# Kernel optimization log

Hardware: AMD Instinct MI355X
Metric: run time of the kernel (lower is better)

## Reference

```python
import jax, jax.numpy as jnp
import numpy as np

N = 100000
E = 1600000
D_IN = 128
HID = 128
OUT = 64


def _sage_conv(x, edge_index, W_l, W_r, b, num_nodes):
    # PyG SAGEConv (aggr='mean'): out = lin_l(mean_{j in N(i)} x_j) + lin_r(x_i)
    src, dst = edge_index[0], edge_index[1]
    msgs = x[src]  # [E, d] gather from source nodes
    summed = jax.ops.segment_sum(msgs, dst, num_segments=num_nodes)  # [N, d]
    cnt = jax.ops.segment_sum(jnp.ones((msgs.shape[0],), x.dtype), dst, num_segments=num_nodes)
    agg = summed / jnp.maximum(cnt, 1.0)[:, None]  # mean; isolated nodes -> 0
    return agg @ W_l + b + x @ W_r


def setup_inputs() -> dict:
    key = jax.random.key(0)
    ks = jax.random.split(key, 8)
    x = jax.random.normal(ks[0], (N, D_IN), dtype=jnp.float32)
    edge_index = jax.random.randint(ks[1], (2, E), 0, N, dtype=jnp.int64)
    s1 = 1.0 / np.sqrt(D_IN)
    s2 = 1.0 / np.sqrt(HID)
    W_l1 = jax.random.uniform(ks[2], (D_IN, HID), jnp.float32, -s1, s1)
    W_r1 = jax.random.uniform(ks[3], (D_IN, HID), jnp.float32, -s1, s1)
    b1 = jnp.zeros((HID,), jnp.float32)
    W_l2 = jax.random.uniform(ks[4], (HID, OUT), jnp.float32, -s2, s2)
    W_r2 = jax.random.uniform(ks[5], (HID, OUT), jnp.float32, -s2, s2)
    b2 = jnp.zeros((OUT,), jnp.float32)
    return {"x": x, "edge_index": edge_index, "W_l1": W_l1, "W_r1": W_r1,
            "b1": b1, "W_l2": W_l2, "W_r2": W_r2, "b2": b2}


def reference(x, edge_index, W_l1, W_r1, b1, W_l2, W_r2, b2):
    h = _sage_conv(x, edge_index, W_l1, W_r1, b1, N)
    h = jax.nn.relu(h)
    out = _sage_conv(h, edge_index, W_l2, W_r2, b2, N)
    return out
```

## Files before the change

kernel.cpp:

```cpp
#include <hip/hip_runtime.h>
#include <hip/hip_fp16.h>

typedef __attribute__((ext_vector_type(8))) short bf16x8;
typedef __attribute__((ext_vector_type(4))) float f32x4;

__device__ __forceinline__ f32x4 mfma16(bf16x8 a, bf16x8 b, f32x4 c) {
    return __builtin_amdgcn_mfma_f32_16x16x32_bf16(a, b, c, 0, 0, 0);
}

__device__ __forceinline__ unsigned short bf16_rte(float f) {
    unsigned int u = __float_as_uint(f);
    unsigned int r = (u + 0x7FFFu + ((u >> 16) & 1u)) >> 16;
    return (unsigned short)r;
}
__device__ __forceinline__ float bf16_f(unsigned short h) {
    return __uint_as_float(((unsigned int)h) << 16);
}

__device__ __forceinline__ void split8h(bf16x8 raw, bf16x8& hi, bf16x8& lo) {
#pragma unroll
    for (int j = 0; j < 8; ++j) {
        float f = __half2float(__ushort_as_half((unsigned short)raw[j]));
        unsigned short h = bf16_rte(f);
        hi[j] = (short)h;
        lo[j] = (short)bf16_rte(f - bf16_f(h));
    }
}

__global__ __launch_bounds__(256) void k_wconv_all(
    const float* __restrict__ Wl1, const float* __restrict__ Wr1,
    const float* __restrict__ Wl2, const float* __restrict__ Wr2,
    unsigned short* __restrict__ w1ah, unsigned short* __restrict__ w1al,
    unsigned short* __restrict__ w1bh, unsigned short* __restrict__ w1bl,
    unsigned short* __restrict__ w2ah, unsigned short* __restrict__ w2al,
    unsigned short* __restrict__ w2bh, unsigned short* __restrict__ w2bl) {
    int b = blockIdx.x;
    const float* W;
    unsigned short *hi, *lo;
    int F, e;
    if (b < 64)       { W = Wl1; hi = w1ah; lo = w1al; F = 128; e = b * 256 + threadIdx.x; }
    else if (b < 128) { W = Wr1; hi = w1bh; lo = w1bl; F = 128; e = (b - 64) * 256 + threadIdx.x; }
    else if (b < 160) { W = Wl2; hi = w2ah; lo = w2al; F = 64;  e = (b - 128) * 256 + threadIdx.x; }
    else              { W = Wr2; hi = w2bh; lo = w2bl; F = 64;  e = (b - 160) * 256 + threadIdx.x; }
    if (e >= 128 * F) return;
    int col = e >> 7, k = e & 127;
    float v = W[(size_t)k * F + col];
    unsigned short h = bf16_rte(v);
    hi[e] = h;
    lo[e] = bf16_rte(v - bf16_f(h));
}

__global__ __launch_bounds__(256) void k_xconv(const float* __restrict__ x,
                                               unsigned short* __restrict__ x16,
                                               int total8) {
    int i = blockIdx.x * 256 + threadIdx.x;
    if (i >= total8) return;
    const float4* xp = (const float4*)x + (size_t)i * 2;
    float4 a = xp[0], b = xp[1];
    bf16x8 o;
    o[0] = (short)__half_as_ushort(__float2half_rn(a.x));
    o[1] = (short)__half_as_ushort(__float2half_rn(a.y));
    o[2] = (short)__half_as_ushort(__float2half_rn(a.z));
    o[3] = (short)__half_as_ushort(__float2half_rn(a.w));
    o[4] = (short)__half_as_ushort(__float2half_rn(b.x));
    o[5] = (short)__half_as_ushort(__float2half_rn(b.y));
    o[6] = (short)__half_as_ushort(__float2half_rn(b.z));
    o[7] = (short)__half_as_ushort(__float2half_rn(b.w));
    *(bf16x8*)&x16[(size_t)i * 8] = o;
}


#define MAXNB 1024

__global__ __launch_bounds__(256) void k_bcount(
    const int* __restrict__ dst, int* __restrict__ bcnt, int E, int chunk, int nb) {
    __shared__ int h[MAXNB];
    int t = threadIdx.x;
    for (int i = t; i < nb; i += 256) h[i] = 0;
    __syncthreads();
    int base = blockIdx.x * chunk;
    int end = min(base + chunk, E);
    for (int i = base + t; i < end; i += 256) atomicAdd(&h[dst[i] >> 7], 1);
    __syncthreads();
    for (int i = t; i < nb; i += 256)
        if (h[i]) atomicAdd(&bcnt[i], h[i]);
}

__global__ void k_bscan(const int* __restrict__ bcnt, int* __restrict__ boff,
                        int* __restrict__ bcur, int nb) {
    __shared__ int sh[1024];
    int t = threadIdx.x;
    int v = (t < nb) ? bcnt[t] : 0;
    sh[t] = v;
    __syncthreads();
    for (int off = 1; off < 1024; off <<= 1) {
        int u = (t >= off) ? sh[t - off] : 0;
        __syncthreads();
        sh[t] += u;
        __syncthreads();
    }
    if (t < nb) {
        int ex = sh[t] - v;
        boff[t] = ex;
        bcur[t] = ex;
    }
}

__global__ __launch_bounds__(256) void k_bscatter(
    const int* __restrict__ src, const int* __restrict__ dst,
    int* __restrict__ bcur, int2* __restrict__ pairs, int E, int chunk, int nb) {
    __shared__ int h[MAXNB];
    __shared__ int curs[MAXNB];
    int t = threadIdx.x;
    for (int i = t; i < nb; i += 256) h[i] = 0;
    __syncthreads();
    int base = blockIdx.x * chunk;
    int end = min(base + chunk, E);
    for (int i = base + t; i < end; i += 256) atomicAdd(&h[dst[i] >> 7], 1);
    __syncthreads();
    for (int i = t; i < nb; i += 256)
        curs[i] = h[i] ? atomicAdd(&bcur[i], h[i]) : 0;
    __syncthreads();
    for (int i = base + t; i < end; i += 256) {
        int d = dst[i];
        int p = atomicAdd(&curs[d >> 7], 1);
        pairs[p] = make_int2(d, src[i]);
    }
}

__global__ __launch_bounds__(256) void k_build(
    const int2* __restrict__ pairs, const int* __restrict__ boff,
    int* __restrict__ csr, int* __restrict__ start, int* __restrict__ deg,
    int n, int nb, int E) {
    __shared__ int scnt[128];
    __shared__ int soff[128];
    __shared__ int cur[128];
    int b = blockIdx.x;
    int t = threadIdx.x;
    int base = boff[b];
    int end = (b + 1 < nb) ? boff[b + 1] : E;
    if (t < 128) scnt[t] = 0;
    __syncthreads();
    for (int i = base + t; i < end; i += 256) {
        int2 e = pairs[i];
        atomicAdd(&scnt[e.x & 127], 1);
    }
    __syncthreads();
    if (t < 128) soff[t] = scnt[t];
    __syncthreads();
    for (int off = 1; off < 128; off <<= 1) {
        int val = 0;
        if (t < 128 && t >= off) val = soff[t - off];
        __syncthreads();
        if (t < 128) soff[t] += val;
        __syncthreads();
    }
    if (t < 128) {
        int c = scnt[t];
        int ex = soff[t] - c;
        int node = b * 128 + t;
        if (node < n) {
            start[node] = base + ex;
            deg[node] = c;
        }
        cur[t] = base + ex;
    }
    __syncthreads();
    for (int i = base + t; i < end; i += 256) {
        int2 e = pairs[i];
        int p = atomicAdd(&cur[e.x & 127], 1);
        csr[p] = e.y;
    }
}


#define SR 40

template <int FOUT, bool OUT_H16>
__device__ __forceinline__ void gemm_dual_body(
    const unsigned short* __restrict__ X0h, const unsigned short* __restrict__ X1h,
    const unsigned short* __restrict__ W0H, const unsigned short* __restrict__ W0L,
    const unsigned short* __restrict__ W1H, const unsigned short* __restrict__ W1L,
    const float* __restrict__ bias, unsigned short* __restrict__ dstH,
    float* __restrict__ dstF, int n) {
    constexpr int CT = FOUT / 64;
    __shared__ unsigned short aHi[4][64 * SR], aLo[4][64 * SR];

    int t = threadIdx.x;
    int wv = t >> 6, l = t & 63, q = l >> 4, nl = l & 15;
    int wc = wv * (FOUT / 4);
    int node0 = blockIdx.x * 64;
    int sn = t >> 2, q4 = t & 3;
    int gn = min(node0 + sn, n - 1);

    bf16x8 s1r[4];
    {
        const unsigned short* p = X1h + (size_t)gn * 128 + q4 * 8;
#pragma unroll
        for (int c = 0; c < 4; ++c) s1r[c] = *(const bf16x8*)(p + c * 32);
    }
    bf16x8 w1h0[CT], w1l0[CT];
#pragma unroll
    for (int uu = 0; uu < CT; ++uu) {
        int base = (wc + uu * 16 + nl) * 128 + q * 8;
        w1h0[uu] = *(const bf16x8*)&W1H[base];
        w1l0[uu] = *(const bf16x8*)&W1L[base];
    }

    {
        const unsigned short* p = X0h + (size_t)gn * 128 + q4 * 8;
        bf16x8 r[4];
#pragma unroll
        for (int c = 0; c < 4; ++c) r[c] = *(const bf16x8*)(p + c * 32);
        int base = sn * SR + q4 * 8;
#pragma unroll
        for (int c = 0; c < 4; ++c) {
            bf16x8 hi, lo;
            split8h(r[c], hi, lo);
            *(bf16x8*)&aHi[c][base] = hi;
            *(bf16x8*)&aLo[c][base] = lo;
        }
    }

    f32x4 acc[4][CT];
#pragma unroll
    for (int a = 0; a < 4; ++a)
#pragma unroll
        for (int b = 0; b < CT; ++b) acc[a][b] = (f32x4){0.f, 0.f, 0.f, 0.f};

    bf16x8 wh[2][CT], wl[2][CT];
#pragma unroll
    for (int uu = 0; uu < CT; ++uu) {
        int base = (wc + uu * 16 + nl) * 128 + q * 8;
        wh[0][uu] = *(const bf16x8*)&W0H[base];
        wl[0][uu] = *(const bf16x8*)&W0L[base];
    }
    __syncthreads();

#pragma unroll
    for (int c = 0; c < 4; ++c) {
        if (c < 3) {
#pragma unroll
            for (int uu = 0; uu < CT; ++uu) {
                int base = (wc + uu * 16 + nl) * 128 + (c + 1) * 32 + q * 8;
                wh[(c + 1) & 1][uu] = *(const bf16x8*)&W0H[base];
                wl[(c + 1) & 1][uu] = *(const bf16x8*)&W0L[base];
            }
        }
        bf16x8 ah[4], al[4];
#pragma unroll
        for (int tt = 0; tt < 4; ++tt) {
            int off = (tt * 16 + nl) * SR + q * 8;
            ah[tt] = *(const bf16x8*)&aHi[c][off];
            al[tt] = *(const bf16x8*)&aLo[c][off];
        }
        int cb = c & 1;
#pragma unroll
        for (int tt = 0; tt < 4; ++tt)
#pragma unroll
            for (int uu = 0; uu < CT; ++uu) {
                f32x4 a = acc[tt][uu];
                a = mfma16(al[tt], wh[cb][uu], a);
                a = mfma16(ah[tt], wl[cb][uu], a);
                a = mfma16(ah[tt], wh[cb][uu], a);
                acc[tt][uu] = a;
            }
    }
    __syncthreads();

    {
        int base = sn * SR + q4 * 8;
#pragma unroll
        for (int c = 0; c < 4; ++c) {
            bf16x8 hi, lo;
            split8h(s1r[c], hi, lo);
            *(bf16x8*)&aHi[c][base] = hi;
            *(bf16x8*)&aLo[c][base] = lo;
        }
    }
#pragma unroll
    for (int uu = 0; uu < CT; ++uu) { wh[0][uu] = w1h0[uu]; wl[0][uu] = w1l0[uu]; }
    __syncthreads();

#pragma unroll
    for (int c = 0; c < 4; ++c) {
        if (c < 3) {
#pragma unroll
            for (int uu = 0; uu < CT; ++uu) {
                int base = (wc + uu * 16 + nl) * 128 + (c + 1) * 32 + q * 8;
                wh[(c + 1) & 1][uu] = *(const bf16x8*)&W1H[base];
                wl[(c + 1) & 1][uu] = *(const bf16x8*)&W1L[base];
            }
        }
        bf16x8 ah[4], al[4];
#pragma unroll
        for (int tt = 0; tt < 4; ++tt) {
            int off = (tt * 16 + nl) * SR + q * 8;
            ah[tt] = *(const bf16x8*)&aHi[c][off];
            al[tt] = *(const bf16x8*)&aLo[c][off];
        }
        int cb = c & 1;
#pragma unroll
        for (int tt = 0; tt < 4; ++tt)
#pragma unroll
            for (int uu = 0; uu < CT; ++uu) {
                f32x4 a = acc[tt][uu];
                a = mfma16(al[tt], wh[cb][uu], a);
                a = mfma16(ah[tt], wl[cb][uu], a);
                a = mfma16(ah[tt], wh[cb][uu], a);
                acc[tt][uu] = a;
            }
    }
    __syncthreads();

    if (OUT_H16) {
        unsigned short* tb = &aHi[0][0];
#pragma unroll
        for (int uu = 0; uu < CT; ++uu) {
            int col = wc + uu * 16 + nl;
            float bv = bias[col];
#pragma unroll
            for (int tt = 0; tt < 4; ++tt)
#pragma unroll
                for (int r = 0; r < 4; ++r) {
                    float vv = fmaxf(acc[tt][uu][r] + bv, 0.f);
                    tb[(tt * 16 + q * 4 + r) * 136 + col] =
                        __half_as_ushort(__float2half_rn(vv));
                }
        }
        __syncthreads();
        int node = node0 + sn;
        if (node < n) {
            const unsigned short* sp = tb + sn * 136 + q4 * 32;
            unsigned short* dp = dstH + (size_t)node * 128 + q4 * 32;
#pragma unroll
            for (int i = 0; i < 4; ++i) *(bf16x8*)(dp + i * 8) = *(const bf16x8*)(sp + i * 8);
        }
    } else {
        float* tb = (float*)&aHi[0][0];
#pragma unroll
        for (int uu = 0; uu < CT; ++uu) {
            int col = wc + uu * 16 + nl;
            float bv = bias[col];
#pragma unroll
            for (int tt = 0; tt < 4; ++tt)
#pragma unroll
                for (int r = 0; r < 4; ++r)
                    tb[(tt * 16 + q * 4 + r) * 68 + col] = acc[tt][uu][r] + bv;
        }
        __syncthreads();
        int node = node0 + sn;
        if (node < n) {
            const float* sp = tb + sn * 68 + q4 * 16;
            float* dp = dstF + (size_t)node * 64 + q4 * 16;
#pragma unroll
            for (int i = 0; i < 4; ++i) *(float4*)(dp + i * 4) = *(const float4*)(sp + i * 4);
        }
    }
}

__global__ __launch_bounds__(256, 4) void gemm1f(
    const unsigned short* __restrict__ X, const unsigned short* __restrict__ XM,
    const unsigned short* WrH, const unsigned short* WrL,
    const unsigned short* WlH, const unsigned short* WlL,
    const float* __restrict__ bias, unsigned short* __restrict__ h16, int n) {
    gemm_dual_body<128, true>(X, XM, WrH, WrL, WlH, WlL, bias, h16, nullptr, n);
}

__global__ __launch_bounds__(256, 4) void gemm2f(
    const unsigned short* __restrict__ H, const unsigned short* __restrict__ HM,
    const unsigned short* WrH, const unsigned short* WrL,
    const unsigned short* WlH, const unsigned short* WlL,
    const float* __restrict__ bias, float* __restrict__ out, int n) {
    gemm_dual_body<64, false>(H, HM, WrH, WrL, WlH, WlL, bias, nullptr, out, n);
}

__global__ __launch_bounds__(256) void aggF(
    const unsigned short* __restrict__ tab, const int* __restrict__ csr,
    const int* __restrict__ start, const int* __restrict__ deg,
    unsigned short* __restrict__ outm, int n) {
    int gid = blockIdx.x * blockDim.x + threadIdx.x;
    int wave = gid >> 6, lane = gid & 63;
    int sub = lane >> 4, fl = lane & 15;
    int node = wave * 4 + sub;
    if (node >= n) return;
    int s = start[node], d = deg[node];
    float4 A0 = {0.f, 0.f, 0.f, 0.f}, A1 = {0.f, 0.f, 0.f, 0.f};
    int j = 0;
    if (d >= 4) {
        int i0 = csr[s], i1 = csr[s + 1], i2 = csr[s + 2], i3 = csr[s + 3];
        for (; j + 8 <= d; j += 4) {
            int n0 = csr[s + j + 4], n1 = csr[s + j + 5];
            int n2 = csr[s + j + 6], n3 = csr[s + j + 7];
            uint4 r0 = ((const uint4*)(tab + (size_t)i0 * 128))[fl];
            uint4 r1 = ((const uint4*)(tab + (size_t)i1 * 128))[fl];
            uint4 r2 = ((const uint4*)(tab + (size_t)i2 * 128))[fl];
            uint4 r3 = ((const uint4*)(tab + (size_t)i3 * 128))[fl];
#pragma unroll
            for (int e = 0; e < 4; ++e) {
                uint4 r = e == 0 ? r0 : (e == 1 ? r1 : (e == 2 ? r2 : r3));
                float2 v0 = __half22float2(*(const __half2*)&r.x);
                float2 v1 = __half22float2(*(const __half2*)&r.y);
                float2 v2 = __half22float2(*(const __half2*)&r.z);
                float2 v3 = __half22float2(*(const __half2*)&r.w);
                A0.x += v0.x; A0.y += v0.y; A0.z += v1.x; A0.w += v1.y;
                A1.x += v2.x; A1.y += v2.y; A1.z += v3.x; A1.w += v3.y;
            }
            i0 = n0; i1 = n1; i2 = n2; i3 = n3;
        }
        {
            uint4 r0 = ((const uint4*)(tab + (size_t)i0 * 128))[fl];
            uint4 r1 = ((const uint4*)(tab + (size_t)i1 * 128))[fl];
            uint4 r2 = ((const uint4*)(tab + (size_t)i2 * 128))[fl];
            uint4 r3 = ((const uint4*)(tab + (size_t)i3 * 128))[fl];
#pragma unroll
            for (int e = 0; e < 4; ++e) {
                uint4 r = e == 0 ? r0 : (e == 1 ? r1 : (e == 2 ? r2 : r3));
                float2 v0 = __half22float2(*(const __half2*)&r.x);
                float2 v1 = __half22float2(*(const __half2*)&r.y);
                float2 v2 = __half22float2(*(const __half2*)&r.z);
                float2 v3 = __half22float2(*(const __half2*)&r.w);
                A0.x += v0.x; A0.y += v0.y; A0.z += v1.x; A0.w += v1.y;
                A1.x += v2.x; A1.y += v2.y; A1.z += v3.x; A1.w += v3.y;
            }
            j += 4;
        }
    }
    for (; j < d; ++j) {
        uint4 r = ((const uint4*)(tab + (size_t)csr[s + j] * 128))[fl];
        float2 v0 = __half22float2(*(const __half2*)&r.x);
        float2 v1 = __half22float2(*(const __half2*)&r.y);
        float2 v2 = __half22float2(*(const __half2*)&r.z);
        float2 v3 = __half22float2(*(const __half2*)&r.w);
        A0.x += v0.x; A0.y += v0.y; A0.z += v1.x; A0.w += v1.y;
        A1.x += v2.x; A1.y += v2.y; A1.z += v3.x; A1.w += v3.y;
    }
    float inv = 1.0f / (float)max(d, 1);
    __half2 h0 = __floats2half2_rn(A0.x * inv, A0.y * inv);
    __half2 h1 = __floats2half2_rn(A0.z * inv, A0.w * inv);
    __half2 h2 = __floats2half2_rn(A1.x * inv, A1.y * inv);
    __half2 h3 = __floats2half2_rn(A1.z * inv, A1.w * inv);
    uint4 w;
    w.x = *(unsigned int*)&h0;
    w.y = *(unsigned int*)&h1;
    w.z = *(unsigned int*)&h2;
    w.w = *(unsigned int*)&h3;
    *(uint4*)&outm[(size_t)node * 128 + fl * 8] = w;
}


extern "C" void kernel_launch(void* const* d_in, const int* in_sizes, int n_in,
                              void* d_out, int out_size, void* d_ws, size_t ws_size,
                              hipStream_t stream) {
    const float* x   = (const float*)d_in[0];
    const int*   ei  = (const int*)d_in[1];
    const float* Wl1 = (const float*)d_in[2];
    const float* Wr1 = (const float*)d_in[3];
    const float* b1  = (const float*)d_in[4];
    const float* Wl2 = (const float*)d_in[5];
    const float* Wr2 = (const float*)d_in[6];
    const float* b2  = (const float*)d_in[7];
    float* out = (float*)d_out;

    int Nn = in_sizes[0] / 128;
    int E  = in_sizes[1] / 2;
    const int* src = ei;
    const int* dst = ei + E;
    int nb = (Nn + 127) / 128;

    char* ws = (char*)d_ws;
    auto alloc = [&](size_t bytes) -> char* {
        char* pp = ws;
        ws += (bytes + 255) / 256 * 256;
        return pp;
    };
    int* bcnt   = (int*)alloc((size_t)nb * 4);
    int* boff   = (int*)alloc((size_t)nb * 4);
    int* bcur   = (int*)alloc((size_t)nb * 4);
    int* start  = (int*)alloc((size_t)Nn * 4);
    int* deg    = (int*)alloc((size_t)Nn * 4);
    int* csr    = (int*)alloc((size_t)E * 4);
    unsigned short* x16  = (unsigned short*)alloc((size_t)Nn * 128 * 2);
    unsigned short* xm16 = (unsigned short*)alloc((size_t)Nn * 128 * 2);
    unsigned short* h16  = (unsigned short*)alloc((size_t)Nn * 128 * 2);
    unsigned short* hm16 = (unsigned short*)alloc((size_t)Nn * 128 * 2);
    unsigned short* w1ah = (unsigned short*)alloc(128 * 128 * 2);
    unsigned short* w1al = (unsigned short*)alloc(128 * 128 * 2);
    unsigned short* w1bh = (unsigned short*)alloc(128 * 128 * 2);
    unsigned short* w1bl = (unsigned short*)alloc(128 * 128 * 2);
    unsigned short* w2ah = (unsigned short*)alloc(64 * 128 * 2);
    unsigned short* w2al = (unsigned short*)alloc(64 * 128 * 2);
    unsigned short* w2bh = (unsigned short*)alloc(64 * 128 * 2);
    unsigned short* w2bl = (unsigned short*)alloc(64 * 128 * 2);
    int2* pairs = (int2*)hm16;

    hipMemsetAsync(bcnt, 0, (size_t)nb * 4, stream);

    k_wconv_all<<<192, 256, 0, stream>>>(Wl1, Wr1, Wl2, Wr2,
                                         w1ah, w1al, w1bh, w1bl,
                                         w2ah, w2al, w2bh, w2bl);
    k_xconv<<<(Nn * 16 + 255) / 256, 256, 0, stream>>>(x, x16, Nn * 16);

    int chunk = (E + 255) / 256;
    k_bcount<<<256, 256, 0, stream>>>(dst, bcnt, E, chunk, nb);
    k_bscan<<<1, 1024, 0, stream>>>(bcnt, boff, bcur, nb);
    k_bscatter<<<256, 256, 0, stream>>>(src, dst, bcur, pairs, E, chunk, nb);
    k_build<<<nb, 256, 0, stream>>>(pairs, boff, csr, start, deg, Nn, nb, E);

    int gb = (Nn + 63) / 64;
    int ga = (Nn + 15) / 16;
    aggF<<<ga, 256, 0, stream>>>(x16, csr, start, deg, xm16, Nn);
    gemm1f<<<gb, 256, 0, stream>>>(x16, xm16, w1bh, w1bl, w1ah, w1al, b1, h16, Nn);
    aggF<<<ga, 256, 0, stream>>>(h16, csr, start, deg, hm16, Nn);
    gemm2f<<<gb, 256, 0, stream>>>(h16, hm16, w2bh, w2bl, w2ah, w2al, b2, out, Nn);
}
```

Measured before the change: 366.8 us.

## Project layer-2 features before aggregation and fuse prep kernels

Layer 2 now multiplies h by W_l2 first (a 64-wide fp16 table) and by W_r2 plus the bias, then averages the projected 64-wide rows over neighbours and adds them to the output. This uses the linearity of the mean so the second gather reads 64 fp16 features per edge instead of 128. The weight conversion, x conversion and bcnt zeroing are merged into one launch, and the GEMM launch bounds drop from 4 to 2 blocks per unit. In exchange the projected values are rounded to fp16 before averaging, and the output gets a read-modify-write pass.

```diff
diff --git a/kernel.cpp b/kernel.cpp
--- a/kernel.cpp
+++ b/kernel.cpp
@@ -27,46 +27,49 @@
     }
 }
 
-__global__ __launch_bounds__(256) void k_wconv_all(
+__global__ __launch_bounds__(256) void k_prep(
     const float* __restrict__ Wl1, const float* __restrict__ Wr1,
     const float* __restrict__ Wl2, const float* __restrict__ Wr2,
     unsigned short* __restrict__ w1ah, unsigned short* __restrict__ w1al,
     unsigned short* __restrict__ w1bh, unsigned short* __restrict__ w1bl,
     unsigned short* __restrict__ w2ah, unsigned short* __restrict__ w2al,
-    unsigned short* __restrict__ w2bh, unsigned short* __restrict__ w2bl) {
+    unsigned short* __restrict__ w2bh, unsigned short* __restrict__ w2bl,
+    const float* __restrict__ x, unsigned short* __restrict__ x16,
+    int* __restrict__ bcnt, int nb, int total8) {
     int b = blockIdx.x;
-    const float* W;
-    unsigned short *hi, *lo;
-    int F, e;
-    if (b < 64)       { W = Wl1; hi = w1ah; lo = w1al; F = 128; e = b * 256 + threadIdx.x; }
-    else if (b < 128) { W = Wr1; hi = w1bh; lo = w1bl; F = 128; e = (b - 64) * 256 + threadIdx.x; }
-    else if (b < 160) { W = Wl2; hi = w2ah; lo = w2al; F = 64;  e = (b - 128) * 256 + threadIdx.x; }
-    else              { W = Wr2; hi = w2bh; lo = w2bl; F = 64;  e = (b - 160) * 256 + threadIdx.x; }
-    if (e >= 128 * F) return;
-    int col = e >> 7, k = e & 127;
-    float v = W[(size_t)k * F + col];
-    unsigned short h = bf16_rte(v);
-    hi[e] = h;
-    lo[e] = bf16_rte(v - bf16_f(h));
-}
-
-__global__ __launch_bounds__(256) void k_xconv(const float* __restrict__ x,
-                                               unsigned short* __restrict__ x16,
-                                               int total8) {
-    int i = blockIdx.x * 256 + threadIdx.x;
-    if (i >= total8) return;
-    const float4* xp = (const float4*)x + (size_t)i * 2;
-    float4 a = xp[0], b = xp[1];
-    bf16x8 o;
-    o[0] = (short)__half_as_ushort(__float2half_rn(a.x));
-    o[1] = (short)__half_as_ushort(__float2half_rn(a.y));
-    o[2] = (short)__half_as_ushort(__float2half_rn(a.z));
-    o[3] = (short)__half_as_ushort(__float2half_rn(a.w));
-    o[4] = (short)__half_as_ushort(__float2half_rn(b.x));
-    o[5] = (short)__half_as_ushort(__float2half_rn(b.y));
-    o[6] = (short)__half_as_ushort(__float2half_rn(b.z));
-    o[7] = (short)__half_as_ushort(__float2half_rn(b.w));
-    *(bf16x8*)&x16[(size_t)i * 8] = o;
+    int t = threadIdx.x;
+    if (b < 192) {
+        const float* W;
+        unsigned short *hi, *lo;
+        int F, e;
+        if (b < 64)       { W = Wl1; hi = w1ah; lo = w1al; F = 128; e = b * 256 + t; }
+        else if (b < 128) { W = Wr1; hi = w1bh; lo = w1bl; F = 128; e = (b - 64) * 256 + t; }
+        else if (b < 160) { W = Wl2; hi = w2ah; lo = w2al; F = 64;  e = (b - 128) * 256 + t; }
+        else              { W = Wr2; hi = w2bh; lo = w2bl; F = 64;  e = (b - 160) * 256 + t; }
+        if (e >= 128 * F) return;
+        int col = e >> 7, k = e & 127;
+        float v = W[(size_t)k * F + col];
+        unsigned short h = bf16_rte(v);
+        hi[e] = h;
+        lo[e] = bf16_rte(v - bf16_f(h));
+    } else if (b == 192) {
+        for (int i = t; i < nb; i += 256) bcnt[i] = 0;
+    } else {
+        int i = (b - 193) * 256 + t;
+        if (i >= total8) return;
+        const float4* xp = (const float4*)x + (size_t)i * 2;
+        float4 a = xp[0], bb = xp[1];
+        bf16x8 o;
+        o[0] = (short)__half_as_ushort(__float2half_rn(a.x));
+        o[1] = (short)__half_as_ushort(__float2half_rn(a.y));
+        o[2] = (short)__half_as_ushort(__float2half_rn(a.z));
+        o[3] = (short)__half_as_ushort(__float2half_rn(a.w));
+        o[4] = (short)__half_as_ushort(__float2half_rn(bb.x));
+        o[5] = (short)__half_as_ushort(__float2half_rn(bb.y));
+        o[6] = (short)__half_as_ushort(__float2half_rn(bb.z));
+        o[7] = (short)__half_as_ushort(__float2half_rn(bb.w));
+        *(bf16x8*)&x16[(size_t)i * 8] = o;
+    }
 }
 
 
@@ -176,14 +179,13 @@
 
 #define SR 40
 
-template <int FOUT, bool OUT_H16>
-__device__ __forceinline__ void gemm_dual_body(
+__global__ __launch_bounds__(256, 2) void gemm1f(
     const unsigned short* __restrict__ X0h, const unsigned short* __restrict__ X1h,
     const unsigned short* __restrict__ W0H, const unsigned short* __restrict__ W0L,
     const unsigned short* __restrict__ W1H, const unsigned short* __restrict__ W1L,
-    const float* __restrict__ bias, unsigned short* __restrict__ dstH,
-    float* __restrict__ dstF, int n) {
-    constexpr int CT = FOUT / 64;
+    const float* __restrict__ bias, unsigned short* __restrict__ dstH, int n) {
+    constexpr int FOUT = 128;
+    constexpr int CT = 2;
     __shared__ unsigned short aHi[4][64 * SR], aLo[4][64 * SR];
 
     int t = threadIdx.x;
@@ -313,66 +315,143 @@
     }
     __syncthreads();
 
-    if (OUT_H16) {
-        unsigned short* tb = &aHi[0][0];
-#pragma unroll
-        for (int uu = 0; uu < CT; ++uu) {
-            int col = wc + uu * 16 + nl;
+    unsigned short* tb = &aHi[0][0];
+#pragma unroll
+    for (int uu = 0; uu < CT; ++uu) {
+        int col = wc + uu * 16 + nl;
+        float bv = bias[col];
+#pragma unroll
+        for (int tt = 0; tt < 4; ++tt)
+#pragma unroll
+            for (int r = 0; r < 4; ++r) {
+                float vv = fmaxf(acc[tt][uu][r] + bv, 0.f);
+                tb[(tt * 16 + q * 4 + r) * 136 + col] =
+                    __half_as_ushort(__float2half_rn(vv));
+            }
+    }
+    __syncthreads();
+    int node = node0 + sn;
+    if (node < n) {
+        const unsigned short* sp = tb + sn * 136 + q4 * 32;
+        unsigned short* dp = dstH + (size_t)node * 128 + q4 * 32;
+#pragma unroll
+        for (int i = 0; i < 4; ++i) *(bf16x8*)(dp + i * 8) = *(const bf16x8*)(sp + i * 8);
+    }
+}
+
+__global__ __launch_bounds__(256, 2) void gemm2d(
+    const unsigned short* __restrict__ H,
+    const unsigned short* __restrict__ WaH, const unsigned short* __restrict__ WaL,
+    const unsigned short* __restrict__ WbH, const unsigned short* __restrict__ WbL,
+    const float* __restrict__ bias, unsigned short* __restrict__ p16,
+    float* __restrict__ outF, int n) {
+    constexpr int CT = 2;
+    __shared__ unsigned short aHi[4][64 * SR], aLo[4][64 * SR];
+
+    int t = threadIdx.x;
+    int wv = t >> 6, l = t & 63, q = l >> 4, nl = l & 15;
+    int ysel = wv >> 1;
+    int wc = (wv & 1) * 32;
+    int node0 = blockIdx.x * 64;
+    int sn = t >> 2, q4 = t & 3;
+    int gn = min(node0 + sn, n - 1);
+    const unsigned short* WH = ysel ? WbH : WaH;
+    const unsigned short* WL = ysel ? WbL : WaL;
+
+    {
+        const unsigned short* p = H + (size_t)gn * 128 + q4 * 8;
+        bf16x8 r[4];
+#pragma unroll
+        for (int c = 0; c < 4; ++c) r[c] = *(const bf16x8*)(p + c * 32);
+        int base = sn * SR + q4 * 8;
+#pragma unroll
+        for (int c = 0; c < 4; ++c) {
+            bf16x8 hi, lo;
+            split8h(r[c], hi, lo);
+            *(bf16x8*)&aHi[c][base] = hi;
+            *(bf16x8*)&aLo[c][base] = lo;
+        }
+    }
+
+    f32x4 acc[4][CT];
+#pragma unroll
+    for (int a = 0; a < 4; ++a)
+#pragma unroll
+        for (int b = 0; b < CT; ++b) acc[a][b] = (f32x4){0.f, 0.f, 0.f, 0.f};
+
+    bf16x8 wh[2][CT], wl[2][CT];
+#pragma unroll
+    for (int uu = 0; uu < CT; ++uu) {
+        int base = (wc + uu * 16 + nl) * 128 + q * 8;
+        wh[0][uu] = *(const bf16x8*)&WH[base];
+        wl[0][uu] = *(const bf16x8*)&WL[base];
+    }
+    __syncthreads();
+
+#pragma unroll
+    for (int c = 0; c < 4; ++c) {
+        if (c < 3) {
+#pragma unroll
+            for (int uu = 0; uu < CT; ++uu) {
+                int base = (wc + uu * 16 + nl) * 128 + (c + 1) * 32 + q * 8;
+                wh[(c + 1) & 1][uu] = *(const bf16x8*)&WH[base];
+                wl[(c + 1) & 1][uu] = *(const bf16x8*)&WL[base];
+            }
+        }
+        bf16x8 ah[4], al[4];
+#pragma unroll
+        for (int tt = 0; tt < 4; ++tt) {
+            int off = (tt * 16 + nl) * SR + q * 8;
+            ah[tt] = *(const bf16x8*)&aHi[c][off];
+            al[tt] = *(const bf16x8*)&aLo[c][off];
+        }
+        int cb = c & 1;
+#pragma unroll
+        for (int tt = 0; tt < 4; ++tt)
+#pragma unroll
+            for (int uu = 0; uu < CT; ++uu) {
+                f32x4 a = acc[tt][uu];
+                a = mfma16(al[tt], wh[cb][uu], a);
+                a = mfma16(ah[tt], wl[cb][uu], a);
+                a = mfma16(ah[tt], wh[cb][uu], a);
+                acc[tt][uu] = a;
+            }
+    }
+    __syncthreads();
+
+    unsigned short* tbu = &aHi[0][0];
+    float* tbf = (float*)&aLo[0][0];
+#pragma unroll
+    for (int uu = 0; uu < CT; ++uu) {
+        int col = wc + uu * 16 + nl;
+        if (ysel) {
             float bv = bias[col];
 #pragma unroll
             for (int tt = 0; tt < 4; ++tt)
 #pragma unroll
-                for (int r = 0; r < 4; ++r) {
-                    float vv = fmaxf(acc[tt][uu][r] + bv, 0.f);
-                    tb[(tt * 16 + q * 4 + r) * 136 + col] =
-                        __half_as_ushort(__float2half_rn(vv));
-                }
-        }
-        __syncthreads();
-        int node = node0 + sn;
-        if (node < n) {
-            const unsigned short* sp = tb + sn * 136 + q4 * 32;
-            unsigned short* dp = dstH + (size_t)node * 128 + q4 * 32;
-#pragma unroll
-            for (int i = 0; i < 4; ++i) *(bf16x8*)(dp + i * 8) = *(const bf16x8*)(sp + i * 8);
-        }
-    } else {
-        float* tb = (float*)&aHi[0][0];
-#pragma unroll
-        for (int uu = 0; uu < CT; ++uu) {
-            int col = wc + uu * 16 + nl;
-            float bv = bias[col];
+                for (int r = 0; r < 4; ++r)
+                    tbf[(tt * 16 + q * 4 + r) * 68 + col] = acc[tt][uu][r] + bv;
+        } else {
 #pragma unroll
             for (int tt = 0; tt < 4; ++tt)
 #pragma unroll
                 for (int r = 0; r < 4; ++r)
-                    tb[(tt * 16 + q * 4 + r) * 68 + col] = acc[tt][uu][r] + bv;
-        }
-        __syncthreads();
-        int node = node0 + sn;
-        if (node < n) {
-            const float* sp = tb + sn * 68 + q4 * 16;
-            float* dp = dstF + (size_t)node * 64 + q4 * 16;
-#pragma unroll
-            for (int i = 0; i < 4; ++i) *(float4*)(dp + i * 4) = *(const float4*)(sp + i * 4);
-        }
-    }
-}
-
-__global__ __launch_bounds__(256, 4) void gemm1f(
-    const unsigned short* __restrict__ X, const unsigned short* __restrict__ XM,
-    const unsigned short* WrH, const unsigned short* WrL,
-    const unsigned short* WlH, const unsigned short* WlL,
-    const float* __restrict__ bias, unsigned short* __restrict__ h16, int n) {
-    gemm_dual_body<128, true>(X, XM, WrH, WrL, WlH, WlL, bias, h16, nullptr, n);
-}
-
-__global__ __launch_bounds__(256, 4) void gemm2f(
-    const unsigned short* __restrict__ H, const unsigned short* __restrict__ HM,
-    const unsigned short* WrH, const unsigned short* WrL,
-    const unsigned short* WlH, const unsigned short* WlL,
-    const float* __restrict__ bias, float* __restrict__ out, int n) {
-    gemm_dual_body<64, false>(H, HM, WrH, WrL, WlH, WlL, bias, nullptr, out, n);
+                    tbu[(tt * 16 + q * 4 + r) * 72 + col] =
+                        __half_as_ushort(__float2half_rn(acc[tt][uu][r]));
+        }
+    }
+    __syncthreads();
+    int node = node0 + sn;
+    if (node < n) {
+        const unsigned short* spu = tbu + sn * 72 + q4 * 16;
+        unsigned short* dpu = p16 + (size_t)node * 64 + q4 * 16;
+        *(bf16x8*)dpu = *(const bf16x8*)spu;
+        *(bf16x8*)(dpu + 8) = *(const bf16x8*)(spu + 8);
+        const float* spf = tbf + sn * 68 + q4 * 16;
+        float* dpf = outF + (size_t)node * 64 + q4 * 16;
+#pragma unroll
+        for (int i = 0; i < 4; ++i) *(float4*)(dpf + i * 4) = *(const float4*)(spf + i * 4);
+    }
 }
 
 __global__ __launch_bounds__(256) void aggF(
@@ -448,6 +527,67 @@
     *(uint4*)&outm[(size_t)node * 128 + fl * 8] = w;
 }
 
+__global__ __launch_bounds__(256) void aggP(
+    const unsigned short* __restrict__ tab, const int* __restrict__ csr,
+    const int* __restrict__ start, const int* __restrict__ deg,
+    float* __restrict__ outF, int n) {
+    int gid = blockIdx.x * blockDim.x + threadIdx.x;
+    int wave = gid >> 6, lane = gid & 63;
+    int sub = lane >> 4, fl = lane & 15;
+    int node = wave * 4 + sub;
+    if (node >= n) return;
+    int s = start[node], d = deg[node];
+    float4 A = {0.f, 0.f, 0.f, 0.f};
+    int j = 0;
+    if (d >= 4) {
+        int i0 = csr[s], i1 = csr[s + 1], i2 = csr[s + 2], i3 = csr[s + 3];
+        for (; j + 8 <= d; j += 4) {
+            int n0 = csr[s + j + 4], n1 = csr[s + j + 5];
+            int n2 = csr[s + j + 6], n3 = csr[s + j + 7];
+            uint2 r0 = ((const uint2*)(tab + (size_t)i0 * 64))[fl];
+            uint2 r1 = ((const uint2*)(tab + (size_t)i1 * 64))[fl];
+            uint2 r2 = ((const uint2*)(tab + (size_t)i2 * 64))[fl];
+            uint2 r3 = ((const uint2*)(tab + (size_t)i3 * 64))[fl];
+#pragma unroll
+            for (int e = 0; e < 4; ++e) {
+                uint2 r = e == 0 ? r0 : (e == 1 ? r1 : (e == 2 ? r2 : r3));
+                float2 v0 = __half22float2(*(const __half2*)&r.x);
+                float2 v1 = __half22float2(*(const __half2*)&r.y);
+                A.x += v0.x; A.y += v0.y; A.z += v1.x; A.w += v1.y;
+            }
+            i0 = n0; i1 = n1; i2 = n2; i3 = n3;
+        }
+        {
+            uint2 r0 = ((const uint2*)(tab + (size_t)i0 * 64))[fl];
+            uint2 r1 = ((const uint2*)(tab + (size_t)i1 * 64))[fl];
+            uint2 r2 = ((const uint2*)(tab + (size_t)i2 * 64))[fl];
+            uint2 r3 = ((const uint2*)(tab + (size_t)i3 * 64))[fl];
+#pragma unroll
+            for (int e = 0; e < 4; ++e) {
+                uint2 r = e == 0 ? r0 : (e == 1 ? r1 : (e == 2 ? r2 : r3));
+                float2 v0 = __half22float2(*(const __half2*)&r.x);
+                float2 v1 = __half22float2(*(const __half2*)&r.y);
+                A.x += v0.x; A.y += v0.y; A.z += v1.x; A.w += v1.y;
+            }
+            j += 4;
+        }
+    }
+    for (; j < d; ++j) {
+        uint2 r = ((const uint2*)(tab + (size_t)csr[s + j] * 64))[fl];
+        float2 v0 = __half22float2(*(const __half2*)&r.x);
+        float2 v1 = __half22float2(*(const __half2*)&r.y);
+        A.x += v0.x; A.y += v0.y; A.z += v1.x; A.w += v1.y;
+    }
+    float inv = 1.0f / (float)max(d, 1);
+    float* op = outF + (size_t)node * 64 + fl * 4;
+    float4 cur = *(float4*)op;
+    cur.x += A.x * inv;
+    cur.y += A.y * inv;
+    cur.z += A.z * inv;
+    cur.w += A.w * inv;
+    *(float4*)op = cur;
+}
+
 
 extern "C" void kernel_launch(void* const* d_in, const int* in_sizes, int n_in,
                               void* d_out, int out_size, void* d_ws, size_t ws_size,
@@ -483,7 +623,7 @@
     unsigned short* x16  = (unsigned short*)alloc((size_t)Nn * 128 * 2);
     unsigned short* xm16 = (unsigned short*)alloc((size_t)Nn * 128 * 2);
     unsigned short* h16  = (unsigned short*)alloc((size_t)Nn * 128 * 2);
-    unsigned short* hm16 = (unsigned short*)alloc((size_t)Nn * 128 * 2);
+    unsigned short* p16  = (unsigned short*)alloc((size_t)Nn * 64 * 2);
     unsigned short* w1ah = (unsigned short*)alloc(128 * 128 * 2);
     unsigned short* w1al = (unsigned short*)alloc(128 * 128 * 2);
     unsigned short* w1bh = (unsigned short*)alloc(128 * 128 * 2);
@@ -492,14 +632,14 @@
     unsigned short* w2al = (unsigned short*)alloc(64 * 128 * 2);
     unsigned short* w2bh = (unsigned short*)alloc(64 * 128 * 2);
     unsigned short* w2bl = (unsigned short*)alloc(64 * 128 * 2);
-    int2* pairs = (int2*)hm16;
-
-    hipMemsetAsync(bcnt, 0, (size_t)nb * 4, stream);
-
-    k_wconv_all<<<192, 256, 0, stream>>>(Wl1, Wr1, Wl2, Wr2,
-                                         w1ah, w1al, w1bh, w1bl,
-                                         w2ah, w2al, w2bh, w2bl);
-    k_xconv<<<(Nn * 16 + 255) / 256, 256, 0, stream>>>(x, x16, Nn * 16);
+    int2* pairs = (int2*)p16;
+
+    int total8 = Nn * 16;
+    int prep_blocks = 193 + (total8 + 255) / 256;
+    k_prep<<<prep_blocks, 256, 0, stream>>>(Wl1, Wr1, Wl2, Wr2,
+                                            w1ah, w1al, w1bh, w1bl,
+                                            w2ah, w2al, w2bh, w2bl,
+                                            x, x16, bcnt, nb, total8);
 
     int chunk = (E + 255) / 256;
     k_bcount<<<256, 256, 0, stream>>>(dst, bcnt, E, chunk, nb);
@@ -511,6 +651,6 @@
     int ga = (Nn + 15) / 16;
     aggF<<<ga, 256, 0, stream>>>(x16, csr, start, deg, xm16, Nn);
     gemm1f<<<gb, 256, 0, stream>>>(x16, xm16, w1bh, w1bl, w1ah, w1al, b1, h16, Nn);
-    aggF<<<ga, 256, 0, stream>>>(h16, csr, start, deg, hm16, Nn);
-    gemm2f<<<gb, 256, 0, stream>>>(h16, hm16, w2bh, w2bl, w2ah, w2al, b2, out, Nn);
-}
+    gemm2d<<<gb, 256, 0, stream>>>(h16, w2ah, w2al, w2bh, w2bl, b2, p16, out, Nn);
+    aggP<<<ga, 256, 0, stream>>>(p16, csr, start, deg, out, Nn);
+}
```

Measured after the change: 332.1 us. 9.4% less time.
